# Kernel optimization log

Hardware: AMD Instinct MI355X
Metric: run time of the kernel (lower is better)

The kernel has to match this reference:

```python
import jax, jax.numpy as jnp
import numpy as np

H = 48       # query heads
KVH = 8      # kv heads (GQA)
G = H // KVH # groups = 6
D = 128      # head_dim
HID = 6144
ROPE_THETA = 1e6


def setup_inputs() -> dict:
    key = jax.random.key(0)
    k1, k2, k3 = jax.random.split(key, 3)
    x = jax.random.normal(k1, (2, 2048, HID), dtype=jnp.float32)
    Wqkv = jax.random.normal(k2, (8192, HID), dtype=jnp.float32) * 0.02
    Wo = jax.random.normal(k3, (HID, HID), dtype=jnp.float32) * 0.02
    return {"x": x, "Wqkv": Wqkv, "Wo": Wo}


def _rotate_half(u):
    return jnp.concatenate([-u[..., D // 2:], u[..., :D // 2]], axis=-1)


def reference(x, Wqkv, Wo):
    B, S, _ = x.shape
    # fused QKV projection, InternLM2 packed layout [B,S,KVH,2+G,D]
    qkv = jnp.einsum('bsh,oh->bso', x, Wqkv).reshape(B, S, KVH, G + 2, D)
    q = qkv[..., :G, :].reshape(B, S, H, D)   # [B,S,H,D]
    k = qkv[..., G, :]                        # [B,S,KVH,D]
    v = qkv[..., G + 1, :]                    # [B,S,KVH,D]

    # RoPE (rotate-half style, theta=1e6)
    inv_freq = 1.0 / (ROPE_THETA ** (jnp.arange(0, D, 2, dtype=jnp.float32) / D))
    freqs = jnp.outer(jnp.arange(S, dtype=jnp.float32), inv_freq)  # [S, D/2]
    emb = jnp.concatenate([freqs, freqs], axis=-1)                 # [S, D]
    cos = jnp.cos(emb)[None, :, None, :]
    sin = jnp.sin(emb)[None, :, None, :]
    q = q * cos + _rotate_half(q) * sin
    k = k * cos + _rotate_half(k) * sin

    # GQA: expand kv heads to query heads
    k = jnp.repeat(k, G, axis=2)  # [B,S,H,D]
    v = jnp.repeat(v, G, axis=2)

    scale = jnp.float32(1.0 / np.sqrt(D))
    scores = jnp.einsum('bqhd,bkhd->bhqk', q, k) * scale  # [B,H,S,S]
    causal = jnp.tril(jnp.ones((S, S), dtype=bool))
    scores = jnp.where(causal[None, None], scores, jnp.float32(-1e30))
    attn = jax.nn.softmax(scores, axis=-1)
    ctx = jnp.einsum('bhqk,bkhd->bqhd', attn, v).reshape(B, S, HID)
    return jnp.einsum('bsh,oh->bso', ctx, Wo)
```

## Files before the change

kernel.cpp:

```cpp
#include <hip/hip_runtime.h>
#include <stdint.h>
#include <stddef.h>


typedef unsigned short u16;
typedef __attribute__((ext_vector_type(8))) short short8;
typedef __attribute__((ext_vector_type(4))) float f32x4;
typedef __attribute__((ext_vector_type(4))) unsigned short u16x4;

typedef const __attribute__((address_space(1))) void* as1_cvp;
typedef __attribute__((address_space(3))) void* as3_vp;

__device__ __forceinline__ float bf2f(u16 u) {
  union { unsigned int i; float f; } v; v.i = ((unsigned)u) << 16; return v.f;
}
__device__ __forceinline__ u16 f2bf(float f) {
  union { float f; unsigned int i; } v; v.f = f;
  unsigned r = v.i + 0x7FFFu + ((v.i >> 16) & 1u);
  return (u16)(r >> 16);
}
__device__ __forceinline__ void gload_lds16(const void* g, void* l) {
  __builtin_amdgcn_global_load_lds((as1_cvp)g, (as3_vp)l, 16, 0, 0);
}

__global__ __launch_bounds__(256) void k_f2bf(const float* __restrict__ in,
                                              u16* __restrict__ out) {
  size_t i = ((size_t)blockIdx.x * 256 + threadIdx.x) * 4;
  f32x4 v = *(const f32x4*)(in + i);
  u16x4 o;
  o[0] = f2bf(v[0]); o[1] = f2bf(v[1]); o[2] = f2bf(v[2]); o[3] = f2bf(v[3]);
  *(u16x4*)(out + i) = o;
}

__device__ __forceinline__ void stage_region(const u16* __restrict__ G,
                                             int K, int kt,
                                             u16 (* __restrict__ XS)[64],
                                             int rmap, int w, int lane) {
  #pragma unroll
  for (int L = 0; L < 2; ++L) {
    const int g = w * 2 + L;
    int rb;
    if (rmap == 0)      rb = g * 8 + (g >> 3) * 64;
    else if (rmap == 1) rb = 64 + g * 8 + (g >> 3) * 64;
    else if (rmap == 2) rb = (g >> 2) * 64 + (g & 3) * 8;
    else                rb = 32 + (g >> 2) * 64 + (g & 3) * 8;
    const int srow = rb + (lane >> 3);
    const int schunk = ((lane & 7) ^ ((lane >> 3) & 7)) * 8;
    gload_lds16(G + (size_t)srow * K + (size_t)kt * 64 + schunk, &XS[rb][0]);
  }
}

#define LDFRAG(XS, row, ks) \
  (*(const short8*)&XS[row][(((ks) * 32) + lhi * 8) ^ swz])

#define MFMA_Q(af, bf, mb, nb)                                              \
  _Pragma("unroll") for (int mf = 0; mf < 4; ++mf)                          \
  _Pragma("unroll") for (int nf = 0; nf < 2; ++nf)                          \
  _Pragma("unroll") for (int ks = 0; ks < 2; ++ks)                          \
    acc[(mb) + mf][(nb) + nf] = __builtin_amdgcn_mfma_f32_16x16x32_bf16(    \
        af[mf][ks], bf[nf][ks], acc[(mb) + mf][(nb) + nf], 0, 0, 0);

#define GEMM_HALF(H) {                                                      \
  const int tAhi  = (t + 1 + (H) < nkt) ? (t + 1 + (H)) : (nkt - 1);        \
  const int tNext = (t + 2 + (H) < nkt) ? (t + 2 + (H)) : (nkt - 1);        \
  short8 a0[4][2], a1[4][2], b0[2][2], b1[2][2];                            \
          \
  _Pragma("unroll") for (int mf = 0; mf < 4; ++mf) {                        \
    a0[mf][0] = LDFRAG(As[H], wm * 128 + mf * 16 + l16, 0);                 \
    a0[mf][1] = LDFRAG(As[H], wm * 128 + mf * 16 + l16, 1); }               \
  _Pragma("unroll") for (int nf = 0; nf < 2; ++nf) {                        \
    b0[nf][0] = LDFRAG(Bs[H], wn * 64 + nf * 16 + l16, 0);                  \
    b0[nf][1] = LDFRAG(Bs[H], wn * 64 + nf * 16 + l16, 1);                  \
    b1[nf][0] = LDFRAG(Bs[H], wn * 64 + (nf + 2) * 16 + l16, 0);            \
    b1[nf][1] = LDFRAG(Bs[H], wn * 64 + (nf + 2) * 16 + l16, 1); }          \
  stage_region(Ap, K, tAhi, As[1 - (H)], 1, w, lane);                       \
  __builtin_amdgcn_s_barrier();                                             \
  __builtin_amdgcn_s_setprio(1);                                            \
  MFMA_Q(a0, b0, 0, 0);                                                     \
  MFMA_Q(a0, b1, 0, 2);                                                     \
  __builtin_amdgcn_s_setprio(0);                                            \
  __builtin_amdgcn_s_barrier();                                             \
     \
  _Pragma("unroll") for (int mf = 0; mf < 4; ++mf) {                        \
    a1[mf][0] = LDFRAG(As[H], wm * 128 + (mf + 4) * 16 + l16, 0);           \
    a1[mf][1] = LDFRAG(As[H], wm * 128 + (mf + 4) * 16 + l16, 1); }         \
  stage_region(Ap, K, tNext, As[H], 0, w, lane);                            \
  stage_region(Bp, K, tNext, Bs[H], 2, w, lane);                            \
  stage_region(Bp, K, tNext, Bs[H], 3, w, lane);                            \
  asm volatile("s_waitcnt vmcnt(6)" ::: "memory");                          \
  __builtin_amdgcn_s_barrier();                                             \
  __builtin_amdgcn_s_setprio(1);                                            \
  MFMA_Q(a1, b0, 4, 0);                                                     \
  MFMA_Q(a1, b1, 4, 2);                                                     \
  __builtin_amdgcn_s_setprio(0);                                            \
  __builtin_amdgcn_s_barrier();                                             \
}

template<int WRITE_BF16>
__global__ __launch_bounds__(512, 2) void k_gemm256(const u16* __restrict__ A,
                                                    const u16* __restrict__ B,
                                                    void* __restrict__ Cout,
                                                    int M, int N, int K) {
  __shared__ u16 As[2][256][64];
  __shared__ u16 Bs[2][256][64];
  (void)M;
  const int tid  = threadIdx.x;
  const int lane = tid & 63;
  const int w    = tid >> 6;
  const int wm   = w >> 2;
  const int wn   = w & 3;
  const int l16  = lane & 15, lhi = lane >> 4;
  const int swz  = (l16 & 7) << 3;

  const int nbx = gridDim.x;
  int id = blockIdx.y * nbx + blockIdx.x;
  const int cpx = (nbx * gridDim.y) >> 3;
  id = (id & 7) * cpx + (id >> 3);
  const long m0 = (long)(id / nbx) * 256;
  const long n0 = (long)(id % nbx) * 256;

  const u16* Ap = A + (size_t)m0 * K;
  const u16* Bp = B + (size_t)n0 * K;

  f32x4 acc[8][4] = {};
  const int nkt = K >> 6;
  const int niter = nkt >> 1;

  stage_region(Ap, K, 0, As[0], 0, w, lane);
  stage_region(Ap, K, 0, As[0], 1, w, lane);
  stage_region(Bp, K, 0, Bs[0], 2, w, lane);
  stage_region(Bp, K, 0, Bs[0], 3, w, lane);
  stage_region(Ap, K, 1, As[1], 0, w, lane);
  stage_region(Bp, K, 1, Bs[1], 2, w, lane);
  stage_region(Bp, K, 1, Bs[1], 3, w, lane);
  asm volatile("s_waitcnt vmcnt(6)" ::: "memory");
  __builtin_amdgcn_s_barrier();

  for (int i = 0; i < niter; ++i) {
    const int t = 2 * i;
    GEMM_HALF(0)
    GEMM_HALF(1)
  }

  asm volatile("s_waitcnt vmcnt(0)" ::: "memory");
  #pragma unroll
  for (int mf = 0; mf < 8; ++mf)
    #pragma unroll
    for (int nf = 0; nf < 4; ++nf)
      #pragma unroll
      for (int j = 0; j < 4; ++j) {
        const size_t row = m0 + wm * 128 + mf * 16 + lhi * 4 + j;
        const size_t col = n0 + wn * 64 + nf * 16 + l16;
        const float v = acc[mf][nf][j];
        if (WRITE_BF16) ((u16*)Cout)[row * N + col] = f2bf(v);
        else            ((float*)Cout)[row * N + col] = v;
      }
}

__global__ __launch_bounds__(256) void k_rope(const u16* __restrict__ QKV,
                                              u16* __restrict__ Qo,
                                              u16* __restrict__ Ko) {
  const unsigned tid = blockIdx.x * 256 + threadIdx.x;
  const int j    = tid & 63;
  const int slot = (tid >> 6) & 7;
  const int kvh  = (tid >> 9) & 7;
  const int t    = tid >> 12;
  if (slot == 7) return;
  const int b = t >> 11, s = t & 2047;
  const size_t base = (size_t)t * 8192 + kvh * 1024 + slot * 128;
  const float v0 = bf2f(QKV[base + j]);
  const float v1 = bf2f(QKV[base + j + 64]);
  const float invf = __expf(-(float)j * 0.21586735246819181f);
  const float ang = (float)s * invf;
  float sn, cs;
  __sincosf(ang, &sn, &cs);
  const float o0 = v0 * cs - v1 * sn;
  const float o1 = v1 * cs + v0 * sn;
  if (slot < 6) {
    const int hh = kvh * 6 + slot;
    const size_t o = ((size_t)(b * 48 + hh) * 2048 + s) * 128 + j;
    Qo[o] = f2bf(o0); Qo[o + 64] = f2bf(o1);
  } else {
    const size_t o = ((size_t)(b * 8 + kvh) * 2048 + s) * 128 + j;
    Ko[o] = f2bf(o0); Ko[o + 64] = f2bf(o1);
  }
}

__global__ __launch_bounds__(256) void k_vtrans(const u16* __restrict__ QKV,
                                                u16* __restrict__ VT) {
  __shared__ u16 T[64][136];
  const int bid = blockIdx.x;
  const int st  = bid & 31;
  const int kvh = (bid >> 5) & 7;
  const int b   = bid >> 8;
  const int tid = threadIdx.x;
  const int r   = tid >> 4;
  const int c8  = (tid & 15) * 8;
  const size_t qoff = ((size_t)(b * 2048 + st * 64)) * 8192 + kvh * 1024 + 896;
  #pragma unroll
  for (int p = 0; p < 4; ++p) {
    short8 v = *(const short8*)&QKV[qoff + (size_t)(p * 16 + r) * 8192 + c8];
    *(short8*)&T[p * 16 + r][c8] = v;
  }
  __syncthreads();
  const int dd = tid >> 3;
  const int s8 = (tid & 7) * 8;
  const size_t vbase = ((size_t)(b * 8 + kvh) * 128) * 2048 + st * 64;
  #pragma unroll
  for (int p = 0; p < 4; ++p) {
    const int d = p * 32 + dd;
    short8 o;
    #pragma unroll
    for (int i = 0; i < 8; ++i) o[i] = (short)T[s8 + i][d];
    *(short8*)&VT[vbase + (size_t)d * 2048 + s8] = o;
  }
}

__global__ __launch_bounds__(256) void k_attn(const u16* __restrict__ Q,
                                              const u16* __restrict__ Kg,
                                              const u16* __restrict__ VT,
                                              u16* __restrict__ CTX) {
  __shared__ u16 Ks[64][128];
  __shared__ u16 Vs[128][64];
  __shared__ u16 Ps[4][16][64];
  const int bid = blockIdx.x;
  const int qt  = 31 - (bid / 96);
  const int bh  = bid % 96;
  const int h   = bh % 48;
  const int b   = bh / 48;
  const int kvh = h / 6;
  const int tid = threadIdx.x, lane = tid & 63, w = tid >> 6;
  const int l16 = lane & 15, lhi = lane >> 4;
  const int swz = (l16 & 7) << 3;
  const float SC = 0.08838834764831845f;

  short8 qf[4];
  {
    const size_t qrow = ((size_t)(b * 48 + h) * 2048 + qt * 64 + w * 16 + l16) * 128;
    #pragma unroll
    for (int kc = 0; kc < 4; ++kc)
      qf[kc] = *(const short8*)&Q[qrow + kc * 32 + lhi * 8];
  }
  f32x4 cacc[8] = {};
  float m_r[4], l_r[4];
  #pragma unroll
  for (int j = 0; j < 4; ++j) { m_r[j] = -1e30f; l_r[j] = 0.f; }

  const u16* Kb = Kg + (size_t)(b * 8 + kvh) * 2048 * 128;
  const u16* Vb = VT + (size_t)(b * 8 + kvh) * 128 * 2048;

  for (int kt = 0; kt <= qt; ++kt) {
    #pragma unroll
    for (int c = 0; c < 4; ++c) {
      const int krow = w * 16 + c * 4 + lhi;
      const int kcol = (l16 * 8) ^ ((krow & 7) << 3);
      gload_lds16(&Kb[(size_t)(kt * 64 + krow) * 128 + kcol], &Ks[w * 16 + c * 4][0]);
      const int vrow = w * 32 + c * 8 + (lane >> 3);
      const int vcol = ((lane & 7) * 8) ^ (((lane >> 3) & 7) << 3);
      gload_lds16(&Vb[(size_t)vrow * 2048 + kt * 64 + vcol], &Vs[w * 32 + c * 8][0]);
    }
    __syncthreads();

    f32x4 sacc[4] = {};
    #pragma unroll
    for (int ni = 0; ni < 4; ++ni)
      #pragma unroll
      for (int kc = 0; kc < 4; ++kc) {
        const short8 kfr = *(const short8*)&Ks[ni * 16 + l16][(kc * 32 + lhi * 8) ^ swz];
        sacc[ni] = __builtin_amdgcn_mfma_f32_16x16x32_bf16(qf[kc], kfr, sacc[ni], 0, 0, 0);
      }

    const bool diag = (kt == qt);
    float sv[4][4], alpha[4];
    #pragma unroll
    for (int j = 0; j < 4; ++j) {
      const int rloc = w * 16 + lhi * 4 + j;
      float mx = -1e30f;
      #pragma unroll
      for (int ni = 0; ni < 4; ++ni) {
        float s = sacc[ni][j] * SC;
        if (diag && (ni * 16 + l16 > rloc)) s = -1e30f;
        sv[ni][j] = s;
        mx = fmaxf(mx, s);
      }
      mx = fmaxf(mx, __shfl_xor(mx, 1, 16));
      mx = fmaxf(mx, __shfl_xor(mx, 2, 16));
      mx = fmaxf(mx, __shfl_xor(mx, 4, 16));
      mx = fmaxf(mx, __shfl_xor(mx, 8, 16));
      const float mnew = fmaxf(m_r[j], mx);
      alpha[j] = __expf(m_r[j] - mnew);
      float rs = 0.f;
      #pragma unroll
      for (int ni = 0; ni < 4; ++ni) {
        const float p = __expf(sv[ni][j] - mnew);
        sv[ni][j] = p;
        rs += p;
      }
      rs += __shfl_xor(rs, 1, 16);
      rs += __shfl_xor(rs, 2, 16);
      rs += __shfl_xor(rs, 4, 16);
      rs += __shfl_xor(rs, 8, 16);
      l_r[j] = l_r[j] * alpha[j] + rs;
      m_r[j] = mnew;
    }
    #pragma unroll
    for (int ni = 0; ni < 4; ++ni)
      #pragma unroll
      for (int j = 0; j < 4; ++j)
        Ps[w][lhi * 4 + j][(ni * 16 + l16) ^ (((lhi * 4 + j) & 7) << 3)] = f2bf(sv[ni][j]);
    #pragma unroll
    for (int nb = 0; nb < 8; ++nb)
      #pragma unroll
      for (int j = 0; j < 4; ++j)
        cacc[nb][j] *= alpha[j];
    #pragma unroll
    for (int kc2 = 0; kc2 < 2; ++kc2) {
      const short8 pa = *(const short8*)&Ps[w][l16][(kc2 * 32 + lhi * 8) ^ swz];
      #pragma unroll
      for (int nb = 0; nb < 8; ++nb) {
        const short8 vfr = *(const short8*)&Vs[nb * 16 + l16][(kc2 * 32 + lhi * 8) ^ swz];
        cacc[nb] = __builtin_amdgcn_mfma_f32_16x16x32_bf16(pa, vfr, cacc[nb], 0, 0, 0);
      }
    }
    __syncthreads();
  }

  const size_t crow = (size_t)(b * 2048 + qt * 64 + w * 16);
  #pragma unroll
  for (int nb = 0; nb < 8; ++nb)
    #pragma unroll
    for (int j = 0; j < 4; ++j) {
      const float v = cacc[nb][j] / l_r[j];
      CTX[(crow + lhi * 4 + j) * 6144 + h * 128 + nb * 16 + l16] = f2bf(v);
    }
}

extern "C" void kernel_launch(void* const* d_in, const int* in_sizes, int n_in,
                              void* d_out, int out_size, void* d_ws, size_t ws_size,
                              hipStream_t stream) {
  const float* x    = (const float*)d_in[0];
  const float* wqkv = (const float*)d_in[1];
  const float* wo   = (const float*)d_in[2];
  float* out = (float*)d_out;
  char* ws = (char*)d_ws;

  u16* xb  = (u16*)(ws);
  u16* wqb = (u16*)(ws + 50331648UL);
  u16* wob = (u16*)(ws + 150994944UL);
  u16* qkv = (u16*)(ws + 226492416UL);
  u16* Qb  = (u16*)(ws + 293601280UL);
  u16* Kb  = (u16*)(ws + 343932928UL);
  u16* VTb = (u16*)(ws + 352321536UL);
  u16* ctx = (u16*)(ws + 360710144UL);

  k_f2bf<<<25165824 / 1024, 256, 0, stream>>>(x, xb);
  k_f2bf<<<50331648 / 1024, 256, 0, stream>>>(wqkv, wqb);
  k_f2bf<<<37748736 / 1024, 256, 0, stream>>>(wo, wob);

  k_gemm256<1><<<dim3(8192 / 256, 4096 / 256), 512, 0, stream>>>(
      xb, wqb, qkv, 4096, 8192, 6144);

  k_rope<<<16777216 / 256, 256, 0, stream>>>(qkv, Qb, Kb);
  k_vtrans<<<512, 256, 0, stream>>>(qkv, VTb);

  k_attn<<<2 * 48 * 32, 256, 0, stream>>>(Qb, Kb, VTb, ctx);

  k_gemm256<0><<<dim3(6144 / 256, 4096 / 256), 512, 0, stream>>>(
      ctx, wob, out, 4096, 6144, 6144);
}
```

Before: 1.080 ms.

## Double attention query tile to 128 rows per block to reuse K/V tiles

Each attention block now processes 128 query rows (32 per wave, as two 16-row MFMA subtiles) instead of 64, so every K/V tile loaded into LDS feeds twice as many MFMAs. The grid is halved and the causal mask is generalized to cover the last two key tiles. This cuts global and LDS traffic per unit of compute, at the cost of more registers per thread (two accumulator sets), possible lower occupancy, and fewer blocks for load balancing.

```diff
diff --git a/kernel.cpp b/kernel.cpp
--- a/kernel.cpp
+++ b/kernel.cpp
@@ -222,9 +222,9 @@
                                               u16* __restrict__ CTX) {
   __shared__ u16 Ks[64][128];
   __shared__ u16 Vs[128][64];
-  __shared__ u16 Ps[4][16][64];
+  __shared__ u16 Ps[4][32][64];
   const int bid = blockIdx.x;
-  const int qt  = 31 - (bid / 96);
+  const int qt  = 15 - (bid / 96);
   const int bh  = bid % 96;
   const int h   = bh % 48;
   const int b   = bh / 48;
@@ -234,22 +234,27 @@
   const int swz = (l16 & 7) << 3;
   const float SC = 0.08838834764831845f;
 
-  short8 qf[4];
-  {
-    const size_t qrow = ((size_t)(b * 48 + h) * 2048 + qt * 64 + w * 16 + l16) * 128;
+  short8 qf[2][4];
+  #pragma unroll
+  for (int q2 = 0; q2 < 2; ++q2) {
+    const size_t qrow =
+        ((size_t)(b * 48 + h) * 2048 + qt * 128 + w * 32 + q2 * 16 + l16) * 128;
     #pragma unroll
     for (int kc = 0; kc < 4; ++kc)
-      qf[kc] = *(const short8*)&Q[qrow + kc * 32 + lhi * 8];
-  }
-  f32x4 cacc[8] = {};
-  float m_r[4], l_r[4];
-  #pragma unroll
-  for (int j = 0; j < 4; ++j) { m_r[j] = -1e30f; l_r[j] = 0.f; }
+      qf[q2][kc] = *(const short8*)&Q[qrow + kc * 32 + lhi * 8];
+  }
+  f32x4 cacc[2][8] = {};
+  float m_r[2][4], l_r[2][4];
+  #pragma unroll
+  for (int q2 = 0; q2 < 2; ++q2)
+    #pragma unroll
+    for (int j = 0; j < 4; ++j) { m_r[q2][j] = -1e30f; l_r[q2][j] = 0.f; }
 
   const u16* Kb = Kg + (size_t)(b * 8 + kvh) * 2048 * 128;
   const u16* Vb = VT + (size_t)(b * 8 + kvh) * 128 * 2048;
 
-  for (int kt = 0; kt <= qt; ++kt) {
+  const int ktmax = 2 * qt + 1;
+  for (int kt = 0; kt <= ktmax; ++kt) {
     #pragma unroll
     for (int c = 0; c < 4; ++c) {
       const int krow = w * 16 + c * 4 + lhi;
@@ -261,78 +266,89 @@
     }
     __syncthreads();
 
-    f32x4 sacc[4] = {};
+    f32x4 sacc[2][4] = {};
     #pragma unroll
     for (int ni = 0; ni < 4; ++ni)
       #pragma unroll
       for (int kc = 0; kc < 4; ++kc) {
         const short8 kfr = *(const short8*)&Ks[ni * 16 + l16][(kc * 32 + lhi * 8) ^ swz];
-        sacc[ni] = __builtin_amdgcn_mfma_f32_16x16x32_bf16(qf[kc], kfr, sacc[ni], 0, 0, 0);
-      }
-
-    const bool diag = (kt == qt);
-    float sv[4][4], alpha[4];
-    #pragma unroll
-    for (int j = 0; j < 4; ++j) {
-      const int rloc = w * 16 + lhi * 4 + j;
-      float mx = -1e30f;
-      #pragma unroll
-      for (int ni = 0; ni < 4; ++ni) {
-        float s = sacc[ni][j] * SC;
-        if (diag && (ni * 16 + l16 > rloc)) s = -1e30f;
-        sv[ni][j] = s;
-        mx = fmaxf(mx, s);
-      }
-      mx = fmaxf(mx, __shfl_xor(mx, 1, 16));
-      mx = fmaxf(mx, __shfl_xor(mx, 2, 16));
-      mx = fmaxf(mx, __shfl_xor(mx, 4, 16));
-      mx = fmaxf(mx, __shfl_xor(mx, 8, 16));
-      const float mnew = fmaxf(m_r[j], mx);
-      alpha[j] = __expf(m_r[j] - mnew);
-      float rs = 0.f;
-      #pragma unroll
-      for (int ni = 0; ni < 4; ++ni) {
-        const float p = __expf(sv[ni][j] - mnew);
-        sv[ni][j] = p;
-        rs += p;
-      }
-      rs += __shfl_xor(rs, 1, 16);
-      rs += __shfl_xor(rs, 2, 16);
-      rs += __shfl_xor(rs, 4, 16);
-      rs += __shfl_xor(rs, 8, 16);
-      l_r[j] = l_r[j] * alpha[j] + rs;
-      m_r[j] = mnew;
+        sacc[0][ni] = __builtin_amdgcn_mfma_f32_16x16x32_bf16(qf[0][kc], kfr, sacc[0][ni], 0, 0, 0);
+        sacc[1][ni] = __builtin_amdgcn_mfma_f32_16x16x32_bf16(qf[1][kc], kfr, sacc[1][ni], 0, 0, 0);
+      }
+
+    const bool diag = (kt >= 2 * qt);
+    #pragma unroll
+    for (int q2 = 0; q2 < 2; ++q2) {
+      float sv[4][4], alpha[4];
+      #pragma unroll
+      for (int j = 0; j < 4; ++j) {
+        const int rloc = w * 32 + q2 * 16 + lhi * 4 + j;
+        float mx = -1e30f;
+        #pragma unroll
+        for (int ni = 0; ni < 4; ++ni) {
+          float s = sacc[q2][ni][j] * SC;
+          if (diag && (kt * 64 + ni * 16 + l16 > qt * 128 + rloc)) s = -1e30f;
+          sv[ni][j] = s;
+          mx = fmaxf(mx, s);
+        }
+        mx = fmaxf(mx, __shfl_xor(mx, 1, 16));
+        mx = fmaxf(mx, __shfl_xor(mx, 2, 16));
+        mx = fmaxf(mx, __shfl_xor(mx, 4, 16));
+        mx = fmaxf(mx, __shfl_xor(mx, 8, 16));
+        const float mnew = fmaxf(m_r[q2][j], mx);
+        alpha[j] = __expf(m_r[q2][j] - mnew);
+        float rs = 0.f;
+        #pragma unroll
+        for (int ni = 0; ni < 4; ++ni) {
+          const float p = __expf(sv[ni][j] - mnew);
+          sv[ni][j] = p;
+          rs += p;
+        }
+        rs += __shfl_xor(rs, 1, 16);
+        rs += __shfl_xor(rs, 2, 16);
+        rs += __shfl_xor(rs, 4, 16);
+        rs += __shfl_xor(rs, 8, 16);
+        l_r[q2][j] = l_r[q2][j] * alpha[j] + rs;
+        m_r[q2][j] = mnew;
+      }
+      #pragma unroll
+      for (int ni = 0; ni < 4; ++ni)
+        #pragma unroll
+        for (int j = 0; j < 4; ++j)
+          Ps[w][q2 * 16 + lhi * 4 + j]
+            [(ni * 16 + l16) ^ (((lhi * 4 + j) & 7) << 3)] = f2bf(sv[ni][j]);
+      #pragma unroll
+      for (int nb = 0; nb < 8; ++nb)
+        #pragma unroll
+        for (int j = 0; j < 4; ++j)
+          cacc[q2][nb][j] *= alpha[j];
     }
-    #pragma unroll
-    for (int ni = 0; ni < 4; ++ni)
-      #pragma unroll
-      for (int j = 0; j < 4; ++j)
-        Ps[w][lhi * 4 + j][(ni * 16 + l16) ^ (((lhi * 4 + j) & 7) << 3)] = f2bf(sv[ni][j]);
-    #pragma unroll
-    for (int nb = 0; nb < 8; ++nb)
-      #pragma unroll
-      for (int j = 0; j < 4; ++j)
-        cacc[nb][j] *= alpha[j];
+
     #pragma unroll
     for (int kc2 = 0; kc2 < 2; ++kc2) {
-      const short8 pa = *(const short8*)&Ps[w][l16][(kc2 * 32 + lhi * 8) ^ swz];
+      const short8 pa0 = *(const short8*)&Ps[w][l16][(kc2 * 32 + lhi * 8) ^ swz];
+      const short8 pa1 = *(const short8*)&Ps[w][16 + l16][(kc2 * 32 + lhi * 8) ^ swz];
       #pragma unroll
       for (int nb = 0; nb < 8; ++nb) {
         const short8 vfr = *(const short8*)&Vs[nb * 16 + l16][(kc2 * 32 + lhi * 8) ^ swz];
-        cacc[nb] = __builtin_amdgcn_mfma_f32_16x16x32_bf16(pa, vfr, cacc[nb], 0, 0, 0);
+        cacc[0][nb] = __builtin_amdgcn_mfma_f32_16x16x32_bf16(pa0, vfr, cacc[0][nb], 0, 0, 0);
+        cacc[1][nb] = __builtin_amdgcn_mfma_f32_16x16x32_bf16(pa1, vfr, cacc[1][nb], 0, 0, 0);
       }
     }
     __syncthreads();
   }
 
-  const size_t crow = (size_t)(b * 2048 + qt * 64 + w * 16);
-  #pragma unroll
-  for (int nb = 0; nb < 8; ++nb)
-    #pragma unroll
-    for (int j = 0; j < 4; ++j) {
-      const float v = cacc[nb][j] / l_r[j];
-      CTX[(crow + lhi * 4 + j) * 6144 + h * 128 + nb * 16 + l16] = f2bf(v);
-    }
+  #pragma unroll
+  for (int q2 = 0; q2 < 2; ++q2) {
+    const size_t crow = (size_t)(b * 2048 + qt * 128 + w * 32 + q2 * 16);
+    #pragma unroll
+    for (int nb = 0; nb < 8; ++nb)
+      #pragma unroll
+      for (int j = 0; j < 4; ++j) {
+        const float v = cacc[q2][nb][j] / l_r[q2][j];
+        CTX[(crow + lhi * 4 + j) * 6144 + h * 128 + nb * 16 + l16] = f2bf(v);
+      }
+  }
 }
 
 extern "C" void kernel_launch(void* const* d_in, const int* in_sizes, int n_in,
@@ -363,7 +379,7 @@
   k_rope<<<16777216 / 256, 256, 0, stream>>>(qkv, Qb, Kb);
   k_vtrans<<<512, 256, 0, stream>>>(qkv, VTb);
 
-  k_attn<<<2 * 48 * 32, 256, 0, stream>>>(Qb, Kb, VTb, ctx);
+  k_attn<<<2 * 48 * 16, 256, 0, stream>>>(Qb, Kb, VTb, ctx);
 
   k_gemm256<0><<<dim3(6144 / 256, 4096 / 256), 512, 0, stream>>>(
       ctx, wob, out, 4096, 6144, 6144);
```

New measurement: 1.186 ms. +9.9%, slower.
